# Optimization experiments

Hardware: AMD Instinct MI355X
Metric: run time of the kernel (lower is better)

The kernel has to match this reference:

```python
import jax, jax.numpy as jnp
import numpy as np

S = 30.0
ML = 0.4
MS = 0.1
N, D, C = 8192, 1024, 10240

def setup_inputs() -> dict:
    key = jax.random.key(0)
    k1, k2, k3 = jax.random.split(key, 3)
    x = jax.random.normal(k1, (N, D), dtype=jnp.float32)
    labels = jax.random.randint(k2, (N,), 0, C, dtype=jnp.int64)
    # xavier_uniform for weight (C, D)
    limit = float(np.sqrt(6.0 / (C + D)))
    weight = jax.random.uniform(k3, (C, D), dtype=jnp.float32, minval=-limit, maxval=limit)
    return {"x": x, "labels": labels, "weight": weight}

def _l2norm(v, axis):
    # matches F.normalize (eps=1e-12)
    n = jnp.sqrt(jnp.sum(v * v, axis=axis, keepdims=True))
    return v / jnp.maximum(n, 1e-12)

def reference(x, labels, weight):
    # cosine logits, clamped to [-1, 1]
    wf = jnp.clip(_l2norm(x, 1) @ _l2norm(weight, 1).T, -1.0, 1.0)  # (N, C)
    # per-sample additive margin: ml if label<=5 (real) else ms (fake)
    m = jnp.where(labels <= 5, ML, MS).astype(wf.dtype)  # (N,)
    target = jnp.take_along_axis(wf, labels[:, None], axis=1)[:, 0]  # wf[i, labels[i]]
    numerator = S * (target - m)
    # sum over j != label of exp(s*wf[i,j]) == full sum minus the label term
    exp_all = jnp.exp(S * wf)
    excl_sum = jnp.sum(exp_all, axis=1) - jnp.exp(S * target)
    denominator = jnp.exp(numerator) + excl_sum
    L = numerator - jnp.log(denominator)
    return -jnp.mean(L)
```

## Files before the change

### kernel.cpp

```cpp
#include <hip/hip_runtime.h>
#include <hip/hip_bf16.h>

#define N_ROWS 8192
#define DIM    1024
#define NCLS   10240
#define S_SCALE 30.0f
#define M_LARGE 0.4f
#define M_SMALL 0.1f

typedef __attribute__((ext_vector_type(4))) int   i32x4;

#define GLD16(gp, lp) __builtin_amdgcn_global_load_lds( \
    (const __attribute__((address_space(1))) unsigned int*)(gp), \
    (__attribute__((address_space(3))) unsigned int*)(lp), 16, 0, 0)

__global__ void prep_kernel(const float* __restrict__ x, const float* __restrict__ w,
                            float* __restrict__ inv_x, float* __restrict__ inv_w,
                            float* __restrict__ fx, float* __restrict__ fw,
                            float* __restrict__ gsum,
                            signed char* __restrict__ xq, signed char* __restrict__ wq){
    int b = blockIdx.x;
    bool isx = (b < N_ROWS);
    int r = isx ? b : b - N_ROWS;
    const float4* src = (const float4*)((isx ? x : w) + (size_t)r * DIM);
    float4 v = src[threadIdx.x];
    float ss = v.x*v.x + v.y*v.y + v.z*v.z + v.w*v.w;
    float am = fmaxf(fmaxf(fabsf(v.x), fabsf(v.y)), fmaxf(fabsf(v.z), fabsf(v.w)));
    #pragma unroll
    for (int o = 32; o; o >>= 1){
        ss += __shfl_down(ss, o);
        am  = fmaxf(am, __shfl_down(am, o));
    }
    __shared__ float pss[4], pam[4];
    int lane = threadIdx.x & 63, wid = threadIdx.x >> 6;
    if (lane == 0){ pss[wid] = ss; pam[wid] = am; }
    __syncthreads();
    float t    = pss[0] + pss[1] + pss[2] + pss[3];
    float amax = fmaxf(fmaxf(pam[0], pam[1]), fmaxf(pam[2], pam[3]));
    float inv  = 1.0f / fmaxf(sqrtf(t), 1e-12f);
    float s    = fmaxf(amax, 1e-20f) * (1.0f/127.0f);
    float rs   = 127.0f / fmaxf(amax, 1e-20f);
    int q0 = __float2int_rn(v.x * rs), q1 = __float2int_rn(v.y * rs);
    int q2 = __float2int_rn(v.z * rs), q3 = __float2int_rn(v.w * rs);
    unsigned int pk = (q0 & 0xff) | ((q1 & 0xff) << 8) | ((q2 & 0xff) << 16) | ((q3 & 0xff) << 24);
    ((unsigned int*)((isx ? xq : wq) + (size_t)r * DIM))[threadIdx.x] = pk;
    if (threadIdx.x == 0){
        if (isx){ inv_x[r] = inv; fx[r] = s * inv; gsum[r] = 0.0f; }
        else    { inv_w[r] = inv; fw[r] = s * inv; }
    }
}

__global__ void target_kernel(const float* __restrict__ x, const float* __restrict__ w,
                              const int* __restrict__ labels,
                              const float* __restrict__ inv_x, const float* __restrict__ inv_w,
                              float* __restrict__ tgt){
    int wid = threadIdx.x >> 6, lane = threadIdx.x & 63;
    int i = blockIdx.x * 4 + wid;
    int lab = labels[i];
    const float4* xp = (const float4*)(x + (size_t)i   * DIM);
    const float4* wp = (const float4*)(w + (size_t)lab * DIM);
    float acc = 0.f;
    #pragma unroll
    for (int c = 0; c < 4; ++c){
        float4 a = xp[c*64 + lane];
        float4 b = wp[c*64 + lane];
        acc += a.x*b.x + a.y*b.y + a.z*b.z + a.w*b.w;
    }
    #pragma unroll
    for (int o = 32; o; o >>= 1) acc += __shfl_down(acc, o);
    if (lane == 0){
        float c = acc * inv_x[i] * inv_w[lab];
        c = fminf(fmaxf(c, -1.f), 1.f);
        tgt[i] = c;
    }
}

#define BM 256
#define BN 256
#define BKB 128
#define NT (DIM/BKB)
#define GRID_X (NCLS/BN)
#define GRID_Y (N_ROWS/BM)
#define NWG (GRID_X*GRID_Y)

__global__ __launch_bounds__(512, 2) void gemm_kernel(
        const signed char* __restrict__ xq, const signed char* __restrict__ wq,
        const float* __restrict__ fx, const float* __restrict__ fw,
        float* __restrict__ gsum){
    __shared__ __align__(16) unsigned char As[2][BM*BKB];
    __shared__ __align__(16) unsigned char Bs[2][BN*BKB];
    __shared__ float sumrow[BM];

    int tid = threadIdx.x;
    int bid = blockIdx.x;
    int swz = (bid & 7) * (NWG/8) + (bid >> 3);
    int by = swz / GRID_X, bx = swz % GRID_X;
    int row0 = by * BM, col0 = bx * BN;
    int wid = tid >> 6, lane = tid & 63;
    int wm = wid >> 2, wn = wid & 3;
    int g = lane >> 4, l16 = lane & 15;

    if (tid < BM) sumrow[tid] = 0.f;

    int srow = tid >> 3;
    int csrc = (tid & 7) ^ (srow & 7);
    const signed char* gA = xq + (size_t)(row0 + srow) * DIM + csrc * 16;
    const signed char* gB = wq + (size_t)(col0 + srow) * DIM + csrc * 16;
    int ldso = srow * BKB + (tid & 7) * 16;

    i32x4 acc[8][4] = {};

    #pragma unroll
    for (int h = 0; h < 4; ++h){
        GLD16(gA + (size_t)(h*64)*DIM, &As[0][h*64*BKB + ldso]);
        GLD16(gB + (size_t)(h*64)*DIM, &Bs[0][h*64*BKB + ldso]);
    }
    asm volatile("s_waitcnt vmcnt(0)" ::: "memory");
    __builtin_amdgcn_s_barrier();

    for (int kt = 0; kt < NT; ++kt){
        int b = kt & 1, nb = b ^ 1;
        int knext = (kt + 1) * BKB;
        bool pre = (kt + 1 < NT);
        i32x4 af[4], bfv[4];

        #pragma unroll
        for (int m = 0; m < 4; ++m){
            int r = wm*128 + m*16 + l16;
            af[m] = *(const i32x4*)&As[b][r*BKB + ((g ^ (r & 7)) << 4)];
        }
        #pragma unroll
        for (int n = 0; n < 4; ++n){
            int r = wn*64 + n*16 + l16;
            bfv[n] = *(const i32x4*)&Bs[b][r*BKB + ((g ^ (r & 7)) << 4)];
        }
        if (pre){
            GLD16(gA + knext,                    &As[nb][ldso]);
            GLD16(gA + knext + (size_t)64*DIM,   &As[nb][64*BKB + ldso]);
        }
        __builtin_amdgcn_s_barrier();
        asm volatile("s_waitcnt lgkmcnt(0)" ::: "memory");
        __builtin_amdgcn_sched_barrier(0);
        __builtin_amdgcn_s_setprio(1);
        #pragma unroll
        for (int m = 0; m < 4; ++m)
            #pragma unroll
            for (int n = 0; n < 4; ++n)
                acc[m][n] = __builtin_amdgcn_mfma_i32_16x16x64_i8(af[m], bfv[n], acc[m][n], 0, 0, 0);
        __builtin_amdgcn_s_setprio(0);
        __builtin_amdgcn_s_barrier();

        #pragma unroll
        for (int m = 0; m < 4; ++m){
            int r = wm*128 + (m+4)*16 + l16;
            af[m] = *(const i32x4*)&As[b][r*BKB + ((g ^ (r & 7)) << 4)];
        }
        if (pre){
            GLD16(gA + knext + (size_t)128*DIM,  &As[nb][128*BKB + ldso]);
            GLD16(gA + knext + (size_t)192*DIM,  &As[nb][192*BKB + ldso]);
        }
        __builtin_amdgcn_s_barrier();
        asm volatile("s_waitcnt lgkmcnt(0)" ::: "memory");
        __builtin_amdgcn_sched_barrier(0);
        __builtin_amdgcn_s_setprio(1);
        #pragma unroll
        for (int m = 0; m < 4; ++m)
            #pragma unroll
            for (int n = 0; n < 4; ++n)
                acc[m+4][n] = __builtin_amdgcn_mfma_i32_16x16x64_i8(af[m], bfv[n], acc[m+4][n], 0, 0, 0);
        __builtin_amdgcn_s_setprio(0);
        __builtin_amdgcn_s_barrier();

        #pragma unroll
        for (int m = 0; m < 4; ++m){
            int r = wm*128 + m*16 + l16;
            af[m] = *(const i32x4*)&As[b][r*BKB + (((4+g) ^ (r & 7)) << 4)];
        }
        #pragma unroll
        for (int n = 0; n < 4; ++n){
            int r = wn*64 + n*16 + l16;
            bfv[n] = *(const i32x4*)&Bs[b][r*BKB + (((4+g) ^ (r & 7)) << 4)];
        }
        if (pre){
            GLD16(gB + knext,                    &Bs[nb][ldso]);
            GLD16(gB + knext + (size_t)64*DIM,   &Bs[nb][64*BKB + ldso]);
        }
        __builtin_amdgcn_s_barrier();
        asm volatile("s_waitcnt lgkmcnt(0)" ::: "memory");
        __builtin_amdgcn_sched_barrier(0);
        __builtin_amdgcn_s_setprio(1);
        #pragma unroll
        for (int m = 0; m < 4; ++m)
            #pragma unroll
            for (int n = 0; n < 4; ++n)
                acc[m][n] = __builtin_amdgcn_mfma_i32_16x16x64_i8(af[m], bfv[n], acc[m][n], 0, 0, 0);
        __builtin_amdgcn_s_setprio(0);
        __builtin_amdgcn_s_barrier();

        #pragma unroll
        for (int m = 0; m < 4; ++m){
            int r = wm*128 + (m+4)*16 + l16;
            af[m] = *(const i32x4*)&As[b][r*BKB + (((4+g) ^ (r & 7)) << 4)];
        }
        if (pre){
            GLD16(gB + knext + (size_t)128*DIM,  &Bs[nb][128*BKB + ldso]);
            GLD16(gB + knext + (size_t)192*DIM,  &Bs[nb][192*BKB + ldso]);
        }
        __builtin_amdgcn_s_barrier();
        asm volatile("s_waitcnt lgkmcnt(0)" ::: "memory");
        __builtin_amdgcn_sched_barrier(0);
        __builtin_amdgcn_s_setprio(1);
        #pragma unroll
        for (int m = 0; m < 4; ++m)
            #pragma unroll
            for (int n = 0; n < 4; ++n)
                acc[m+4][n] = __builtin_amdgcn_mfma_i32_16x16x64_i8(af[m], bfv[n], acc[m+4][n], 0, 0, 0);
        __builtin_amdgcn_s_setprio(0);

        asm volatile("s_waitcnt vmcnt(0)" ::: "memory");
        __builtin_amdgcn_sched_barrier(0);
        __builtin_amdgcn_s_barrier();
    }

    float fwv[4];
    #pragma unroll
    for (int n = 0; n < 4; ++n) fwv[n] = fw[col0 + wn*64 + n*16 + l16];
    #pragma unroll
    for (int m = 0; m < 8; ++m){
        #pragma unroll
        for (int rg = 0; rg < 4; ++rg){
            int rl = wm*128 + m*16 + g*4 + rg;
            float fxr = fx[row0 + rl];
            float v = 0.f;
            #pragma unroll
            for (int n = 0; n < 4; ++n){
                float c = (float)acc[m][n][rg] * fxr * fwv[n];
                c = fminf(fmaxf(c, -1.f), 1.f);
                v += __expf(S_SCALE * c);
            }
            v += __shfl_xor(v, 1);
            v += __shfl_xor(v, 2);
            v += __shfl_xor(v, 4);
            v += __shfl_xor(v, 8);
            if (l16 == 0) atomicAdd(&sumrow[rl], v);
        }
    }
    __syncthreads();
    if (tid < BM) atomicAdd(&gsum[row0 + tid], sumrow[tid]);
}

__global__ void finalize_kernel(const float* __restrict__ tgt, const float* __restrict__ gsum,
                                const int* __restrict__ labels, float* __restrict__ out){
    double local = 0.0;
    for (int i = threadIdx.x; i < N_ROWS; i += 256){
        float tv = tgt[i];
        float m  = (labels[i] <= 5) ? M_LARGE : M_SMALL;
        float numer = S_SCALE * (tv - m);
        float excl  = gsum[i] - __expf(S_SCALE * tv);
        float denom = __expf(numer) + excl;
        float L = numer - logf(denom);
        local += (double)L;
    }
    #pragma unroll
    for (int o = 32; o; o >>= 1) local += __shfl_down(local, o);
    __shared__ double part[4];
    int lane = threadIdx.x & 63, wid = threadIdx.x >> 6;
    if (lane == 0) part[wid] = local;
    __syncthreads();
    if (threadIdx.x == 0){
        double s = part[0] + part[1] + part[2] + part[3];
        out[0] = (float)(-s / (double)N_ROWS);
    }
}

extern "C" void kernel_launch(void* const* d_in, const int* in_sizes, int n_in,
                              void* d_out, int out_size, void* d_ws, size_t ws_size,
                              hipStream_t stream) {
    const float* x      = (const float*)d_in[0];
    const int*   labels = (const int*)  d_in[1];
    const float* w      = (const float*)d_in[2];

    float* ws    = (float*)d_ws;
    float* inv_x = ws;
    float* inv_w = inv_x + N_ROWS;
    float* fx    = inv_w + NCLS;
    float* fw    = fx    + N_ROWS;
    float* tgt   = fw    + NCLS;
    float* gsum  = tgt   + N_ROWS;
    signed char* xq = (signed char*)(gsum + N_ROWS);
    signed char* wq = xq + (size_t)N_ROWS * DIM;

    prep_kernel<<<N_ROWS + NCLS, 256, 0, stream>>>(x, w, inv_x, inv_w, fx, fw, gsum, xq, wq);
    target_kernel<<<N_ROWS/4, 256, 0, stream>>>(x, w, labels, inv_x, inv_w, tgt);
    gemm_kernel<<<NWG, 512, 0, stream>>>(xq, wq, fx, fw, gsum);
    finalize_kernel<<<1, 256, 0, stream>>>(tgt, gsum, labels, (float*)d_out);
}
```

Before: 163.1 us.

## Merge GEMM k-loop phases into two larger MFMA batches; widen finalize block

Restructures the int8 GEMM inner loop from four sub-phases (4x4 MFMAs each, with a barrier pair between them) into two phases that each load all 8 A fragments and issue 8x4 MFMAs. The A prefetch is issued in the first phase and the B prefetch in the second. This halves the barrier and wait points per k-step, at the cost of holding 8 A fragments in registers at once. The finalize kernel also moves from 256 to 1024 threads, which shortens its serial loop per thread.

After: 153.2 us. -6.1%, faster.

```diff
diff --git a/kernel.cpp b/kernel.cpp
--- a/kernel.cpp
+++ b/kernel.cpp
@@ -122,10 +122,10 @@
         int b = kt & 1, nb = b ^ 1;
         int knext = (kt + 1) * BKB;
         bool pre = (kt + 1 < NT);
-        i32x4 af[4], bfv[4];
-
-        #pragma unroll
-        for (int m = 0; m < 4; ++m){
+        i32x4 af[8], bfv[4];
+
+        #pragma unroll
+        for (int m = 0; m < 8; ++m){
             int r = wm*128 + m*16 + l16;
             af[m] = *(const i32x4*)&As[b][r*BKB + ((g ^ (r & 7)) << 4)];
         }
@@ -137,13 +137,15 @@
         if (pre){
             GLD16(gA + knext,                    &As[nb][ldso]);
             GLD16(gA + knext + (size_t)64*DIM,   &As[nb][64*BKB + ldso]);
+            GLD16(gA + knext + (size_t)128*DIM,  &As[nb][128*BKB + ldso]);
+            GLD16(gA + knext + (size_t)192*DIM,  &As[nb][192*BKB + ldso]);
         }
         __builtin_amdgcn_s_barrier();
         asm volatile("s_waitcnt lgkmcnt(0)" ::: "memory");
         __builtin_amdgcn_sched_barrier(0);
         __builtin_amdgcn_s_setprio(1);
         #pragma unroll
-        for (int m = 0; m < 4; ++m)
+        for (int m = 0; m < 8; ++m)
             #pragma unroll
             for (int n = 0; n < 4; ++n)
                 acc[m][n] = __builtin_amdgcn_mfma_i32_16x16x64_i8(af[m], bfv[n], acc[m][n], 0, 0, 0);
@@ -151,70 +153,30 @@
         __builtin_amdgcn_s_barrier();
 
         #pragma unroll
-        for (int m = 0; m < 4; ++m){
-            int r = wm*128 + (m+4)*16 + l16;
-            af[m] = *(const i32x4*)&As[b][r*BKB + ((g ^ (r & 7)) << 4)];
+        for (int m = 0; m < 8; ++m){
+            int r = wm*128 + m*16 + l16;
+            af[m] = *(const i32x4*)&As[b][r*BKB + (((4+g) ^ (r & 7)) << 4)];
+        }
+        #pragma unroll
+        for (int n = 0; n < 4; ++n){
+            int r = wn*64 + n*16 + l16;
+            bfv[n] = *(const i32x4*)&Bs[b][r*BKB + (((4+g) ^ (r & 7)) << 4)];
         }
         if (pre){
-            GLD16(gA + knext + (size_t)128*DIM,  &As[nb][128*BKB + ldso]);
-            GLD16(gA + knext + (size_t)192*DIM,  &As[nb][192*BKB + ldso]);
+            GLD16(gB + knext,                    &Bs[nb][ldso]);
+            GLD16(gB + knext + (size_t)64*DIM,   &Bs[nb][64*BKB + ldso]);
+            GLD16(gB + knext + (size_t)128*DIM,  &Bs[nb][128*BKB + ldso]);
+            GLD16(gB + knext + (size_t)192*DIM,  &Bs[nb][192*BKB + ldso]);
         }
         __builtin_amdgcn_s_barrier();
         asm volatile("s_waitcnt lgkmcnt(0)" ::: "memory");
         __builtin_amdgcn_sched_barrier(0);
         __builtin_amdgcn_s_setprio(1);
         #pragma unroll
-        for (int m = 0; m < 4; ++m)
-            #pragma unroll
-            for (int n = 0; n < 4; ++n)
-                acc[m+4][n] = __builtin_amdgcn_mfma_i32_16x16x64_i8(af[m], bfv[n], acc[m+4][n], 0, 0, 0);
-        __builtin_amdgcn_s_setprio(0);
-        __builtin_amdgcn_s_barrier();
-
-        #pragma unroll
-        for (int m = 0; m < 4; ++m){
-            int r = wm*128 + m*16 + l16;
-            af[m] = *(const i32x4*)&As[b][r*BKB + (((4+g) ^ (r & 7)) << 4)];
-        }
-        #pragma unroll
-        for (int n = 0; n < 4; ++n){
-            int r = wn*64 + n*16 + l16;
-            bfv[n] = *(const i32x4*)&Bs[b][r*BKB + (((4+g) ^ (r & 7)) << 4)];
-        }
-        if (pre){
-            GLD16(gB + knext,                    &Bs[nb][ldso]);
-            GLD16(gB + knext + (size_t)64*DIM,   &Bs[nb][64*BKB + ldso]);
-        }
-        __builtin_amdgcn_s_barrier();
-        asm volatile("s_waitcnt lgkmcnt(0)" ::: "memory");
-        __builtin_amdgcn_sched_barrier(0);
-        __builtin_amdgcn_s_setprio(1);
-        #pragma unroll
-        for (int m = 0; m < 4; ++m)
+        for (int m = 0; m < 8; ++m)
             #pragma unroll
             for (int n = 0; n < 4; ++n)
                 acc[m][n] = __builtin_amdgcn_mfma_i32_16x16x64_i8(af[m], bfv[n], acc[m][n], 0, 0, 0);
-        __builtin_amdgcn_s_setprio(0);
-        __builtin_amdgcn_s_barrier();
-
-        #pragma unroll
-        for (int m = 0; m < 4; ++m){
-            int r = wm*128 + (m+4)*16 + l16;
-            af[m] = *(const i32x4*)&As[b][r*BKB + (((4+g) ^ (r & 7)) << 4)];
-        }
-        if (pre){
-            GLD16(gB + knext + (size_t)128*DIM,  &Bs[nb][128*BKB + ldso]);
-            GLD16(gB + knext + (size_t)192*DIM,  &Bs[nb][192*BKB + ldso]);
-        }
-        __builtin_amdgcn_s_barrier();
-        asm volatile("s_waitcnt lgkmcnt(0)" ::: "memory");
-        __builtin_amdgcn_sched_barrier(0);
-        __builtin_amdgcn_s_setprio(1);
-        #pragma unroll
-        for (int m = 0; m < 4; ++m)
-            #pragma unroll
-            for (int n = 0; n < 4; ++n)
-                acc[m+4][n] = __builtin_amdgcn_mfma_i32_16x16x64_i8(af[m], bfv[n], acc[m+4][n], 0, 0, 0);
         __builtin_amdgcn_s_setprio(0);
 
         asm volatile("s_waitcnt vmcnt(0)" ::: "memory");
@@ -252,7 +214,7 @@
 __global__ void finalize_kernel(const float* __restrict__ tgt, const float* __restrict__ gsum,
                                 const int* __restrict__ labels, float* __restrict__ out){
     double local = 0.0;
-    for (int i = threadIdx.x; i < N_ROWS; i += 256){
+    for (int i = threadIdx.x; i < N_ROWS; i += 1024){
         float tv = tgt[i];
         float m  = (labels[i] <= 5) ? M_LARGE : M_SMALL;
         float numer = S_SCALE * (tv - m);
@@ -263,12 +225,14 @@
     }
     #pragma unroll
     for (int o = 32; o; o >>= 1) local += __shfl_down(local, o);
-    __shared__ double part[4];
+    __shared__ double part[16];
     int lane = threadIdx.x & 63, wid = threadIdx.x >> 6;
     if (lane == 0) part[wid] = local;
     __syncthreads();
     if (threadIdx.x == 0){
-        double s = part[0] + part[1] + part[2] + part[3];
+        double s = 0.0;
+        #pragma unroll
+        for (int p = 0; p < 16; ++p) s += part[p];
         out[0] = (float)(-s / (double)N_ROWS);
     }
 }
@@ -293,5 +257,5 @@
     prep_kernel<<<N_ROWS + NCLS, 256, 0, stream>>>(x, w, inv_x, inv_w, fx, fw, gsum, xq, wq);
     target_kernel<<<N_ROWS/4, 256, 0, stream>>>(x, w, labels, inv_x, inv_w, tgt);
     gemm_kernel<<<NWG, 512, 0, stream>>>(xq, wq, fx, fw, gsum);
-    finalize_kernel<<<1, 256, 0, stream>>>(tgt, gsum, labels, (float*)d_out);
-}
+    finalize_kernel<<<1, 1024, 0, stream>>>(tgt, gsum, labels, (float*)d_out);
+}
```
